# Performance work log

Measured on AMD Instinct MI355X. Metric: run time of the kernel, lower is better.

Reference implementation:

```python
import jax, jax.numpy as jnp
import numpy as np

NEG = -1e9

def setup_inputs() -> dict:
    key = jax.random.key(0)
    ks = jax.random.split(key, 6)
    B, T, H = 32, 2048, 1024
    dec = jax.random.normal(ks[0], (B, H), dtype=jnp.float32)
    enc = jax.random.normal(ks[1], (B, T, H), dtype=jnp.float32)
    mask = jax.random.randint(ks[2], (B, T), 0, 2).astype(jnp.int32)
    scale = 1.0 / np.sqrt(H)
    W_enc = jax.random.normal(ks[3], (H, H), dtype=jnp.float32) * scale
    W_dec = jax.random.normal(ks[4], (H, H), dtype=jnp.float32) * scale
    v = jax.random.normal(ks[5], (H,), dtype=jnp.float32) * scale
    return {"decoder_hidden": dec, "encoder_outputs": enc, "mask": mask,
            "W_enc": W_enc, "W_dec": W_dec, "v": v}

def reference(decoder_hidden, encoder_outputs, mask, W_enc, W_dec, v):
    # enc proj: [B,T,H] @ W_enc^T ; dec proj: [B,H] @ W_dec^T broadcast over T
    enc_p = jnp.einsum('bth,oh->bto', encoder_outputs, W_enc)
    dec_p = jnp.einsum('bh,oh->bo', decoder_hidden, W_dec)[:, None, :]  # [B,1,H]
    energy = jnp.tanh(enc_p + dec_p)                                    # [B,T,H]
    scores = jnp.einsum('bth,h->bt', energy, v)                         # [B,T]
    scores = jnp.where(mask == 0, NEG, scores)
    attn_weights = jax.nn.softmax(scores, axis=1)                       # [B,T]
    context = jnp.einsum('bt,bth->bh', attn_weights, encoder_outputs)   # [B,H]
    return (context, attn_weights)
```

## Files before the change

### kernel.cpp

```cpp
#include <hip/hip_runtime.h>
#include <hip/hip_bf16.h>
#include <stdint.h>

#define B_ 32
#define T_ 2048
#define H_ 1024
#define M_ (B_*T_)

typedef __bf16 bf16x8 __attribute__((ext_vector_type(8)));
typedef float  f32x4  __attribute__((ext_vector_type(4)));
typedef float  f32x16 __attribute__((ext_vector_type(16)));

__device__ __forceinline__ float tanh_fast(float x) {
    float e = __expf(2.0f * x);
    return 1.0f - 2.0f / (e + 1.0f);
}

__device__ __forceinline__ bf16x8 cvt2(f32x4 f0, f32x4 f1) {
    bf16x8 h;
    h[0] = (__bf16)f0[0]; h[1] = (__bf16)f0[1]; h[2] = (__bf16)f0[2]; h[3] = (__bf16)f0[3];
    h[4] = (__bf16)f1[0]; h[5] = (__bf16)f1[1]; h[6] = (__bf16)f1[2]; h[7] = (__bf16)f1[3];
    return h;
}

__global__ __launch_bounds__(256) void k_prep(const float* __restrict__ We,
                                              __bf16* __restrict__ Wt,
                                              const float* __restrict__ dec,
                                              const float* __restrict__ Wd,
                                              float* __restrict__ decp) {
    __shared__ float dec8[8][1024];
    int bx = blockIdx.x;
    int tid = threadIdx.x;
    if (bx < 512) {
        int tg = bx * 256 + tid;
        int lane = tg & 63;
        int c = (tg >> 6) & 31;
        int s = tg >> 11;
        int o = c * 32 + (lane & 31);
        int k = s * 16 + (lane >> 5) * 8;
        const f32x4* src = (const f32x4*)&We[(size_t)o * H_ + k];
        *(bf16x8*)&Wt[(size_t)tg * 8] = cvt2(src[0], src[1]);
    } else {
        int bx2 = bx - 512;
        int oc = bx2 >> 2, bg = bx2 & 3;
        int b0 = bg * 8;
        {
            int r = tid >> 5, c4 = (tid & 31) * 4;
            const float* drp = &dec[(size_t)(b0 + r) * H_];
#pragma unroll
            for (int j = 0; j < 8; ++j)
                *(f32x4*)&dec8[r][c4 + j * 128] = *(const f32x4*)&drp[c4 + j * 128];
        }
        __syncthreads();
        int ol = tid & 63, bi = tid >> 6;
        int o = oc * 64 + ol;
        const f32x4* wr = (const f32x4*)&Wd[(size_t)o * H_];
        const f32x4* d0 = (const f32x4*)&dec8[bi][0];
        const f32x4* d1 = (const f32x4*)&dec8[bi + 4][0];
        f32x4 a0 = {0.f,0.f,0.f,0.f}, a1 = {0.f,0.f,0.f,0.f};
#pragma unroll 8
        for (int i = 0; i < 256; ++i) {
            f32x4 wv = wr[i];
            a0 += wv * d0[i];
            a1 += wv * d1[i];
        }
        decp[(b0 + bi) * H_ + o]     = a0[0] + a0[1] + a0[2] + a0[3];
        decp[(b0 + bi + 4) * H_ + o] = a1[0] + a1[1] + a1[2] + a1[3];
    }
}

__global__ __launch_bounds__(256, 3) void k_scores(const float* __restrict__ enc,
                                                   const float* __restrict__ decp,
                                                   const __bf16* __restrict__ Wt,
                                                   const float* __restrict__ v,
                                                   float* __restrict__ scores_p) {
    __shared__ __bf16 A_lds[2][4096];
    __shared__ float red[4][64];

    const int tid = threadIdx.x;
    const int w = tid >> 6, lane = tid & 63;
    const int l5 = lane & 31, q2 = lane >> 5;

    const int bx = blockIdx.x;
    const int xs = bx & 7;
    const int q = bx >> 3;
    const int nt = q & 3;
    const int rg = (q >> 2) * 8 + xs;
    const int m0 = rg * 64;
    const int b = m0 >> 11;
    const int cg0 = nt * 8 + w * 2;

    float dp[2], vvv[2];
#pragma unroll
    for (int ct = 0; ct < 2; ++ct) {
        int col = (cg0 + ct) * 32 + l5;
        dp[ct]  = decp[b * H_ + col];
        vvv[ct] = v[col];
    }

    f32x16 acc[2][2];
#pragma unroll
    for (int rt = 0; rt < 2; ++rt)
#pragma unroll
        for (int ct = 0; ct < 2; ++ct)
#pragma unroll
            for (int g = 0; g < 16; ++g)
                acc[rt][ct][g] = dp[ct];

    const int sr  = w * 16 + (lane >> 2);
    const int slp = lane & 3;
    const float* gsrc = enc + (size_t)(m0 + sr) * H_ + slp * 16;
    const int rtw = sr >> 5, r31 = sr & 31;
    const int wb = ((slp * 2 + rtw) * 64 + (r31 ^ (slp << 2))) * 8;

    {
        f32x4 g0 = *(const f32x4*)(gsrc + 0);
        f32x4 g1 = *(const f32x4*)(gsrc + 4);
        f32x4 g2 = *(const f32x4*)(gsrc + 8);
        f32x4 g3 = *(const f32x4*)(gsrc + 12);
        *(bf16x8*)&A_lds[0][wb]       = cvt2(g0, g1);
        *(bf16x8*)&A_lds[0][wb + 256] = cvt2(g2, g3);
    }

    bf16x8 bb[2][2];
#pragma unroll
    for (int p = 0; p < 2; ++p)
#pragma unroll
        for (int ct = 0; ct < 2; ++ct)
            bb[p][ct] = *(const bf16x8*)&Wt[(((size_t)p * 32 + cg0 + ct) * 64 + lane) * 8];

    __syncthreads();

    int cur = 0;
#pragma unroll 1
    for (int ck = 0; ck < 16; ++ck) {
        f32x4 g0, g1, g2, g3;
        if (ck < 15) {
            const float* gp = gsrc + (ck + 1) * 64;
            g0 = *(const f32x4*)(gp + 0);
            g1 = *(const f32x4*)(gp + 4);
            g2 = *(const f32x4*)(gp + 8);
            g3 = *(const f32x4*)(gp + 12);
        }

        const __bf16* buf = A_lds[cur];

#pragma unroll
        for (int sl = 0; sl < 4; ++sl) {
            const int s = ck * 4 + sl;
            bf16x8 a0 = *(const bf16x8*)&buf[(((sl * 2 + 0) * 64) + q2 * 32 + (l5 ^ (sl << 2))) * 8];
            bf16x8 a1 = *(const bf16x8*)&buf[(((sl * 2 + 1) * 64) + q2 * 32 + (l5 ^ (sl << 2))) * 8];
            bf16x8 w0 = bb[s & 1][0], w1 = bb[s & 1][1];

            {
                int sn = (s + 2) & 63;
#pragma unroll
                for (int ct = 0; ct < 2; ++ct)
                    bb[s & 1][ct] = *(const bf16x8*)&Wt[(((size_t)sn * 32 + cg0 + ct) * 64 + lane) * 8];
            }

            __builtin_amdgcn_s_setprio(1);
            acc[0][0] = __builtin_amdgcn_mfma_f32_32x32x16_bf16(a0, w0, acc[0][0], 0, 0, 0);
            acc[0][1] = __builtin_amdgcn_mfma_f32_32x32x16_bf16(a0, w1, acc[0][1], 0, 0, 0);
            acc[1][0] = __builtin_amdgcn_mfma_f32_32x32x16_bf16(a1, w0, acc[1][0], 0, 0, 0);
            acc[1][1] = __builtin_amdgcn_mfma_f32_32x32x16_bf16(a1, w1, acc[1][1], 0, 0, 0);
            __builtin_amdgcn_s_setprio(0);
        }

        if (ck < 15) {
            __bf16* dst = A_lds[cur ^ 1];
            *(bf16x8*)&dst[wb]       = cvt2(g0, g1);
            *(bf16x8*)&dst[wb + 256] = cvt2(g2, g3);
        }
        __syncthreads();
        cur ^= 1;
    }

    float sp[2][16];
#pragma unroll
    for (int rt = 0; rt < 2; ++rt)
#pragma unroll
        for (int g = 0; g < 16; ++g)
            sp[rt][g] = tanh_fast(acc[rt][0][g]) * vvv[0] + tanh_fast(acc[rt][1][g]) * vvv[1];

#pragma unroll
    for (int rt = 0; rt < 2; ++rt)
#pragma unroll
        for (int g = 0; g < 16; ++g) {
            float s = sp[rt][g];
            s += __shfl_xor(s, 1);
            s += __shfl_xor(s, 2);
            s += __shfl_xor(s, 4);
            s += __shfl_xor(s, 8);
            s += __shfl_xor(s, 16);
            sp[rt][g] = s;
        }

    __syncthreads();
    if (l5 == 0) {
#pragma unroll
        for (int rt = 0; rt < 2; ++rt)
#pragma unroll
            for (int g = 0; g < 16; ++g) {
                int row = rt * 32 + (g & 3) + 8 * (g >> 2) + 4 * q2;
                red[w][row] = sp[rt][g];
            }
    }
    __syncthreads();
    if (tid < 64) {
        float s = red[0][tid] + red[1][tid] + red[2][tid] + red[3][tid];
        scores_p[nt * M_ + m0 + tid] = s;
    }
}

__global__ __launch_bounds__(256) void k_ctx(const float* __restrict__ scores_p,
                                             const int* __restrict__ mask,
                                             const float* __restrict__ enc,
                                             float* __restrict__ attn,
                                             float* __restrict__ ctxp) {
    int bx = blockIdx.x;
    int b = bx >> 4, seg = bx & 15;
    int tid = threadIdx.x;
    int w = tid >> 6, lane = tid & 63;
    __shared__ float sm[2][4];
    __shared__ float wa[128];

    float val[8];
    float mx = -3e38f;
#pragma unroll
    for (int ii = 0; ii < 8; ++ii) {
        int idx = b * T_ + tid + ii * 256;
        float s = scores_p[idx] + scores_p[M_ + idx] + scores_p[2 * M_ + idx] + scores_p[3 * M_ + idx];
        s = (mask[idx] == 0) ? -1e9f : s;
        val[ii] = s;
        mx = fmaxf(mx, s);
    }
#pragma unroll
    for (int m = 1; m <= 32; m <<= 1) mx = fmaxf(mx, __shfl_xor(mx, m));
    if (lane == 0) sm[0][w] = mx;
    __syncthreads();
    mx = fmaxf(fmaxf(sm[0][0], sm[0][1]), fmaxf(sm[0][2], sm[0][3]));
    float lsum = 0.f;
#pragma unroll
    for (int ii = 0; ii < 8; ++ii) {
        val[ii] = __expf(val[ii] - mx);
        lsum += val[ii];
    }
#pragma unroll
    for (int m = 1; m <= 32; m <<= 1) lsum += __shfl_xor(lsum, m);
    if (lane == 0) sm[1][w] = lsum;
    __syncthreads();
    float inv = 1.0f / (sm[1][0] + sm[1][1] + sm[1][2] + sm[1][3]);

    if (seg == 0) {
#pragma unroll
        for (int ii = 0; ii < 8; ++ii)
            attn[b * T_ + tid + ii * 256] = val[ii] * inv;
    }
    {
        int half = seg & 1, ii0 = seg >> 1;
        if ((tid >> 7) == half) wa[tid & 127] = val[ii0] * inv;
    }
    __syncthreads();

    int t0 = seg * 128;
    const float* ep = &enc[((size_t)b * T_ + t0) * H_ + tid * 4];
    f32x4 acc = {0.f, 0.f, 0.f, 0.f};
#pragma unroll 8
    for (int t = 0; t < 128; ++t) {
        float a = wa[t];
        acc += a * *(const f32x4*)(ep + (size_t)t * H_);
    }
    *(f32x4*)&ctxp[((size_t)(seg * B_ + b)) * H_ + tid * 4] = acc;
}

__global__ __launch_bounds__(256) void k_red(const float* __restrict__ ctxp,
                                             float* __restrict__ ctx) {
    int i = blockIdx.x * 256 + threadIdx.x;
    float s = 0.f;
#pragma unroll
    for (int sg = 0; sg < 16; ++sg)
        s += ctxp[(size_t)sg * (B_ * H_) + i];
    ctx[i] = s;
}

extern "C" void kernel_launch(void* const* d_in, const int* in_sizes, int n_in,
                              void* d_out, int out_size, void* d_ws, size_t ws_size,
                              hipStream_t stream) {
    (void)in_sizes; (void)n_in; (void)out_size; (void)ws_size;
    const float* dec  = (const float*)d_in[0];
    const float* enc  = (const float*)d_in[1];
    const int*   mask = (const int*)d_in[2];
    const float* We   = (const float*)d_in[3];
    const float* Wd   = (const float*)d_in[4];
    const float* v    = (const float*)d_in[5];

    float* out = (float*)d_out;
    char* ws = (char*)d_ws;
    float*  decp     = (float*)ws;
    float*  scores_p = (float*)(ws + 131072);
    __bf16* Wt       = (__bf16*)(ws + 131072 + 1048576);
    float*  ctxp     = (float*)(ws + 131072 + 1048576 + 2097152);

    k_prep  <<<576, 256, 0, stream>>>(We, Wt, dec, Wd, decp);
    k_scores<<<4096, 256, 0, stream>>>(enc, decp, Wt, v, scores_p);
    k_ctx   <<<512, 256, 0, stream>>>(scores_p, mask, enc, out + B_ * H_, ctxp);
    k_red   <<<128, 256, 0, stream>>>(ctxp, out);
}
```

Measured before the change: 563.3 us.

## Pre-convert encoder to bf16 MFMA layout and double the row tile per block

Adds a pre-pass that converts the fp32 encoder outputs to bf16 in a pre-swizzled, MFMA-ready layout. The scores GEMM then streams that buffer straight into LDS with global_load_lds, which takes the in-loop fp32 loads and conversions off the critical path. Each block now covers 128 rows instead of 64, so every Wt fragment feeds twice as many MFMAs and half as many blocks are launched. The cost is an extra full write and read of a 128 MB bf16 buffer, plus double the LDS and accumulator registers, which lowers occupancy (launch bounds go from 3 to 2).

```diff
diff --git a/kernel.cpp b/kernel.cpp
--- a/kernel.cpp
+++ b/kernel.cpp
@@ -21,6 +21,12 @@
     h[0] = (__bf16)f0[0]; h[1] = (__bf16)f0[1]; h[2] = (__bf16)f0[2]; h[3] = (__bf16)f0[3];
     h[4] = (__bf16)f1[0]; h[5] = (__bf16)f1[1]; h[6] = (__bf16)f1[2]; h[7] = (__bf16)f1[3];
     return h;
+}
+
+__device__ __forceinline__ void gl_lds16(const __bf16* g, __bf16* l) {
+    __builtin_amdgcn_global_load_lds(
+        (const __attribute__((address_space(1))) void*)g,
+        (__attribute__((address_space(3))) void*)l, 16, 0, 0);
 }
 
 __global__ __launch_bounds__(256) void k_prep(const float* __restrict__ We,
@@ -69,13 +75,33 @@
     }
 }
 
-__global__ __launch_bounds__(256, 3) void k_scores(const float* __restrict__ enc,
+__global__ __launch_bounds__(256) void k_prep_enc(const float* __restrict__ enc,
+                                                  __bf16* __restrict__ enc_t) {
+    int bx = blockIdx.x;
+    int rg2 = bx >> 2, rt = bx & 3;
+    int tid = threadIdx.x;
+    int w = tid >> 6, lane = tid & 63;
+    int r3 = lane >> 3, o3 = lane & 7;
+    int rW = w * 8 + r3;
+    int row = rg2 * 128 + rt * 32 + rW;
+    const float* src = &enc[(size_t)row * H_ + o3 * 8];
+    __bf16* dst = enc_t + (size_t)rg2 * 131072
+                + (((o3 >> 1) * 4 + rt) * 64 + (o3 & 1) * 32 + rW) * 8;
+#pragma unroll 4
+    for (int j = 0; j < 16; ++j) {
+        f32x4 a = *(const f32x4*)(src + j * 64);
+        f32x4 b = *(const f32x4*)(src + j * 64 + 4);
+        *(bf16x8*)&dst[(size_t)j * 8192] = cvt2(a, b);
+    }
+}
+
+__global__ __launch_bounds__(256, 2) void k_scores(const __bf16* __restrict__ enc_t,
                                                    const float* __restrict__ decp,
                                                    const __bf16* __restrict__ Wt,
                                                    const float* __restrict__ v,
                                                    float* __restrict__ scores_p) {
-    __shared__ __bf16 A_lds[2][4096];
-    __shared__ float red[4][64];
+    __shared__ __bf16 A_lds[2][8192];
+    __shared__ float red[4][128];
 
     const int tid = threadIdx.x;
     const int w = tid >> 6, lane = tid & 63;
@@ -85,8 +111,8 @@
     const int xs = bx & 7;
     const int q = bx >> 3;
     const int nt = q & 3;
-    const int rg = (q >> 2) * 8 + xs;
-    const int m0 = rg * 64;
+    const int rg2 = (q >> 2) * 8 + xs;
+    const int m0 = rg2 * 128;
     const int b = m0 >> 11;
     const int cg0 = nt * 8 + w * 2;
 
@@ -98,29 +124,20 @@
         vvv[ct] = v[col];
     }
 
-    f32x16 acc[2][2];
-#pragma unroll
-    for (int rt = 0; rt < 2; ++rt)
+    f32x16 acc[4][2];
+#pragma unroll
+    for (int rt = 0; rt < 4; ++rt)
 #pragma unroll
         for (int ct = 0; ct < 2; ++ct)
 #pragma unroll
             for (int g = 0; g < 16; ++g)
                 acc[rt][ct][g] = dp[ct];
 
-    const int sr  = w * 16 + (lane >> 2);
-    const int slp = lane & 3;
-    const float* gsrc = enc + (size_t)(m0 + sr) * H_ + slp * 16;
-    const int rtw = sr >> 5, r31 = sr & 31;
-    const int wb = ((slp * 2 + rtw) * 64 + (r31 ^ (slp << 2))) * 8;
-
-    {
-        f32x4 g0 = *(const f32x4*)(gsrc + 0);
-        f32x4 g1 = *(const f32x4*)(gsrc + 4);
-        f32x4 g2 = *(const f32x4*)(gsrc + 8);
-        f32x4 g3 = *(const f32x4*)(gsrc + 12);
-        *(bf16x8*)&A_lds[0][wb]       = cvt2(g0, g1);
-        *(bf16x8*)&A_lds[0][wb + 256] = cvt2(g2, g3);
-    }
+    const __bf16* gsrc = enc_t + (size_t)rg2 * 131072 + (size_t)tid * 8;
+
+#pragma unroll
+    for (int i = 0; i < 4; ++i)
+        gl_lds16(gsrc + i * 2048, &A_lds[0][(i * 256 + tid) * 8]);
 
     bf16x8 bb[2][2];
 #pragma unroll
@@ -134,13 +151,12 @@
     int cur = 0;
 #pragma unroll 1
     for (int ck = 0; ck < 16; ++ck) {
-        f32x4 g0, g1, g2, g3;
         if (ck < 15) {
-            const float* gp = gsrc + (ck + 1) * 64;
-            g0 = *(const f32x4*)(gp + 0);
-            g1 = *(const f32x4*)(gp + 4);
-            g2 = *(const f32x4*)(gp + 8);
-            g3 = *(const f32x4*)(gp + 12);
+            const __bf16* gs = gsrc + (size_t)(ck + 1) * 8192;
+            __bf16* dst = A_lds[cur ^ 1];
+#pragma unroll
+            for (int i = 0; i < 4; ++i)
+                gl_lds16(gs + i * 2048, &dst[(i * 256 + tid) * 8]);
         }
 
         const __bf16* buf = A_lds[cur];
@@ -148,8 +164,10 @@
 #pragma unroll
         for (int sl = 0; sl < 4; ++sl) {
             const int s = ck * 4 + sl;
-            bf16x8 a0 = *(const bf16x8*)&buf[(((sl * 2 + 0) * 64) + q2 * 32 + (l5 ^ (sl << 2))) * 8];
-            bf16x8 a1 = *(const bf16x8*)&buf[(((sl * 2 + 1) * 64) + q2 * 32 + (l5 ^ (sl << 2))) * 8];
+            bf16x8 a0 = *(const bf16x8*)&buf[((sl * 4 + 0) * 64 + lane) * 8];
+            bf16x8 a1 = *(const bf16x8*)&buf[((sl * 4 + 1) * 64 + lane) * 8];
+            bf16x8 a2 = *(const bf16x8*)&buf[((sl * 4 + 2) * 64 + lane) * 8];
+            bf16x8 a3 = *(const bf16x8*)&buf[((sl * 4 + 3) * 64 + lane) * 8];
             bf16x8 w0 = bb[s & 1][0], w1 = bb[s & 1][1];
 
             {
@@ -164,27 +182,26 @@
             acc[0][1] = __builtin_amdgcn_mfma_f32_32x32x16_bf16(a0, w1, acc[0][1], 0, 0, 0);
             acc[1][0] = __builtin_amdgcn_mfma_f32_32x32x16_bf16(a1, w0, acc[1][0], 0, 0, 0);
             acc[1][1] = __builtin_amdgcn_mfma_f32_32x32x16_bf16(a1, w1, acc[1][1], 0, 0, 0);
+            acc[2][0] = __builtin_amdgcn_mfma_f32_32x32x16_bf16(a2, w0, acc[2][0], 0, 0, 0);
+            acc[2][1] = __builtin_amdgcn_mfma_f32_32x32x16_bf16(a2, w1, acc[2][1], 0, 0, 0);
+            acc[3][0] = __builtin_amdgcn_mfma_f32_32x32x16_bf16(a3, w0, acc[3][0], 0, 0, 0);
+            acc[3][1] = __builtin_amdgcn_mfma_f32_32x32x16_bf16(a3, w1, acc[3][1], 0, 0, 0);
             __builtin_amdgcn_s_setprio(0);
         }
 
-        if (ck < 15) {
-            __bf16* dst = A_lds[cur ^ 1];
-            *(bf16x8*)&dst[wb]       = cvt2(g0, g1);
-            *(bf16x8*)&dst[wb + 256] = cvt2(g2, g3);
-        }
         __syncthreads();
         cur ^= 1;
     }
 
-    float sp[2][16];
-#pragma unroll
-    for (int rt = 0; rt < 2; ++rt)
+    float sp[4][16];
+#pragma unroll
+    for (int rt = 0; rt < 4; ++rt)
 #pragma unroll
         for (int g = 0; g < 16; ++g)
             sp[rt][g] = tanh_fast(acc[rt][0][g]) * vvv[0] + tanh_fast(acc[rt][1][g]) * vvv[1];
 
 #pragma unroll
-    for (int rt = 0; rt < 2; ++rt)
+    for (int rt = 0; rt < 4; ++rt)
 #pragma unroll
         for (int g = 0; g < 16; ++g) {
             float s = sp[rt][g];
@@ -196,10 +213,9 @@
             sp[rt][g] = s;
         }
 
-    __syncthreads();
     if (l5 == 0) {
 #pragma unroll
-        for (int rt = 0; rt < 2; ++rt)
+        for (int rt = 0; rt < 4; ++rt)
 #pragma unroll
             for (int g = 0; g < 16; ++g) {
                 int row = rt * 32 + (g & 3) + 8 * (g >> 2) + 4 * q2;
@@ -207,7 +223,7 @@
             }
     }
     __syncthreads();
-    if (tid < 64) {
+    if (tid < 128) {
         float s = red[0][tid] + red[1][tid] + red[2][tid] + red[3][tid];
         scores_p[nt * M_ + m0 + tid] = s;
     }
@@ -301,9 +317,11 @@
     float*  scores_p = (float*)(ws + 131072);
     __bf16* Wt       = (__bf16*)(ws + 131072 + 1048576);
     float*  ctxp     = (float*)(ws + 131072 + 1048576 + 2097152);
-
-    k_prep  <<<576, 256, 0, stream>>>(We, Wt, dec, Wd, decp);
-    k_scores<<<4096, 256, 0, stream>>>(enc, decp, Wt, v, scores_p);
-    k_ctx   <<<512, 256, 0, stream>>>(scores_p, mask, enc, out + B_ * H_, ctxp);
-    k_red   <<<128, 256, 0, stream>>>(ctxp, out);
-}
+    __bf16* enc_t    = (__bf16*)(ws + 131072 + 1048576 + 2097152 + 2097152);
+
+    k_prep    <<<576, 256, 0, stream>>>(We, Wt, dec, Wd, decp);
+    k_prep_enc<<<2048, 256, 0, stream>>>(enc, enc_t);
+    k_scores  <<<2048, 256, 0, stream>>>(enc_t, decp, Wt, v, scores_p);
+    k_ctx     <<<512, 256, 0, stream>>>(scores_p, mask, enc, out + B_ * H_, ctxp);
+    k_red     <<<128, 256, 0, stream>>>(ctxp, out);
+}
```

Result: slower. 619.3 us (+9.9%).
